# Kernel optimization log

Measured on AMD Instinct MI355X. Metric: run time of the kernel, lower is better.

The kernel has to match this reference:

```python
import jax, jax.numpy as jnp
import numpy as np

C = 10      # output (digit) capsules
L = 16      # output capsule dim
ROUTING = 3
EPS = 1e-7  # keras backend epsilon


def squash(s):
    # n^2/(1+n^2)/(n+eps) * s, norm over last axis
    n = jnp.linalg.norm(s, axis=-1, keepdims=True)
    return (n ** 2) / (1.0 + n ** 2) / (n + EPS) * s


def setup_inputs() -> dict:
    key = jax.random.key(0)
    k1, k2 = jax.random.split(key)
    B, H, W_, iC, iL = 128, 12, 12, 32, 8
    N = H * W_ * iC  # 4608
    inputs = jax.random.normal(k1, (B, H, W_, iC, iL), dtype=jnp.float32)
    W = jax.random.normal(k2, (N, iL, L * C), dtype=jnp.float32) * 0.05
    biases = jnp.zeros((C, L), dtype=jnp.float32)
    return {"inputs": inputs, "W": W, "biases": biases}


def reference(inputs, W, biases):
    B = inputs.shape[0]
    N = W.shape[0]
    x = inputs.reshape(B, N, -1)                      # [B, N, input_L]
    u = jnp.einsum('bnj,njk->bnk', x, W)              # [B, N, C*L]
    u = u.reshape(B, N, C, L)
    b = jnp.zeros((B, N, C, 1), dtype=u.dtype)
    v = None
    for r in range(ROUTING):
        c = jax.nn.softmax(b, axis=2)                 # over output capsules
        s = jnp.sum(u * c, axis=1, keepdims=True)     # [B, 1, C, L]
        s = s + biases
        v = squash(s)
        if r < ROUTING - 1:
            b = b + jnp.sum(u * v, axis=-1, keepdims=True)
    return v[:, 0]                                    # [B, C, L]
```

## Files before the change

### kernel.cpp

```cpp
#include <hip/hip_runtime.h>
#include <math.h>


namespace {
constexpr int B_   = 128;
constexpr int N_   = 4608;
constexpr int C_   = 10;
constexpr int L_   = 16;
constexpr int CL   = C_ * L_;
constexpr int NCHK = 384;
constexpr int TILE_N = N_ / NCHK;
constexpr int BCL  = B_ * CL;
constexpr int RED_G = 16;
constexpr int RED_K = NCHK / RED_G;
constexpr int WBLK = (N_ * CL) / 256;
constexpr int XBLK = (B_ * N_) / 256;
}

typedef _Float16 h2  __attribute__((ext_vector_type(2)));
typedef _Float16 v4h __attribute__((ext_vector_type(4)));
typedef _Float16 v8h __attribute__((ext_vector_type(8)));
typedef float    v4f __attribute__((ext_vector_type(4)));

__device__ inline h2 pkrtz(float a, float b) {
  return __builtin_bit_cast(h2, __builtin_amdgcn_cvt_pkrtz(a, b));
}

#if defined(__has_builtin)
#if __has_builtin(__builtin_amdgcn_fdot2)
#define HAVE_FDOT2 1
#endif
#endif

__device__ inline float fdot2(h2 a, h2 b, float c) {
#ifdef HAVE_FDOT2
  return __builtin_amdgcn_fdot2(a, b, c, false);
#else
  return c + (float)a[0] * (float)b[0] + (float)a[1] * (float)b[1];
#endif
}

__global__ __launch_bounds__(256)
void conv_pack(const float* __restrict__ W, const float* __restrict__ x,
               v8h* __restrict__ Wt, v8h* __restrict__ xh)
{
  if ((int)blockIdx.x < WBLK) {
    const int t  = blockIdx.x * 256 + threadIdx.x;
    const int n  = t / CL, cl = t % CL;
    const float* p = W + (size_t)n * (8 * CL) + cl;
    v8h o;
#pragma unroll
    for (int j = 0; j < 8; ++j) o[j] = (_Float16)p[j * CL];
    Wt[t] = o;
  } else {
    const int t = ((int)blockIdx.x - WBLK) * 256 + threadIdx.x;
    const float4 a = ((const float4*)x)[(size_t)t * 2 + 0];
    const float4 b = ((const float4*)x)[(size_t)t * 2 + 1];
    v8h o = { (_Float16)a.x, (_Float16)a.y, (_Float16)a.z, (_Float16)a.w,
              (_Float16)b.x, (_Float16)b.y, (_Float16)b.z, (_Float16)b.w };
    xh[t] = o;
  }
}

template<int MODE>
__global__ __launch_bounds__(256, 3)
void pass_kernel(const _Float16* __restrict__ xh,
                 const _Float16* __restrict__ Wt,
                 const float* __restrict__ va,
                 const float* __restrict__ vb,
                 float* __restrict__ partials)
{
  const int lane = threadIdx.x & 63;
  const int wid  = threadIdx.x >> 6;
  const int bl   = lane & 15;
  const int hi   = lane >> 4;
  const int b    = blockIdx.y * 64 + wid * 16 + bl;
  const int n0   = blockIdx.x * TILE_N;
  const int joff = (hi & 1) * 4;
  const int noff = (MODE == 0) ? (hi >> 1) : 0;
  const bool lo  = lane < 32;

  h2 vvh[C_][2];
  if (MODE >= 1) {
#pragma unroll
    for (int c = 0; c < C_; ++c) {
      v4f t = *(const v4f*)(va + ((size_t)b * C_ + c) * L_ + hi * 4);
      if (MODE == 2)
        t += *(const v4f*)(vb + ((size_t)b * C_ + c) * L_ + hi * 4);
      vvh[c][0] = pkrtz(t[0], t[1]);
      vvh[c][1] = pkrtz(t[2], t[3]);
    }
  }

  const v4f zf = {0.f, 0.f, 0.f, 0.f};
  v4f sacc[C_];
#pragma unroll
  for (int c = 0; c < C_; ++c) sacc[c] = zf;

  const _Float16* xp = xh + ((size_t)b * N_ + n0 + noff) * 8 + joff;
  const _Float16* wp = Wt + ((size_t)(n0 + noff) * CL + bl) * 8 + joff;

  constexpr int NSTEP = (MODE == 0) ? 2 : 1;
  for (int nn = 0; nn < TILE_N; nn += NSTEP) {
    v4h xf = *(const v4h*)(xp + nn * 8);
    v4h wf[C_];
#pragma unroll
    for (int c = 0; c < C_; ++c)
      wf[c] = *(const v4h*)(wp + (size_t)nn * (CL * 8) + c * (16 * 8));

    if (MODE == 0) {
#pragma unroll
      for (int c = 0; c < C_; ++c)
        sacc[c] = __builtin_amdgcn_mfma_f32_16x16x16f16(wf[c], xf, sacc[c], 0, 0, 0);
    } else {
      v4h xm = xf;
      if (!lo) { v4h z = {}; xm = z; }

      float tt[C_];
#pragma unroll
      for (int c = 0; c < C_; ++c) {
        const v4f u = __builtin_amdgcn_mfma_f32_16x16x16f16(wf[c], xm, zf, 0, 0, 0);
        const h2 ua = pkrtz(u[0], u[1]);
        const h2 ub = pkrtz(u[2], u[3]);
        float t = fdot2(ua, vvh[c][0], 0.f);
        tt[c] = fdot2(ub, vvh[c][1], t);
      }
#pragma unroll
      for (int c = 0; c < C_; ++c) {
        tt[c] += __shfl_xor(tt[c], 16);
        tt[c] += __shfl_xor(tt[c], 32);
      }
      float es = 0.f;
#pragma unroll
      for (int c = 0; c < C_; ++c) { tt[c] = __expf(tt[c]); es += tt[c]; }
      const float rs = __builtin_amdgcn_rcpf(es);

#pragma unroll
      for (int c = 0; c < C_; ++c) {
        const _Float16 wh = (_Float16)(tt[c] * rs);
        const v4h xw = xm * wh;
        sacc[c] = __builtin_amdgcn_mfma_f32_16x16x16f16(wf[c], xw, sacc[c], 0, 0, 0);
      }
    }
  }

  float* pout = partials + ((size_t)blockIdx.x * B_ + b) * CL + hi * 4;
#pragma unroll
  for (int c = 0; c < C_; ++c)
    *(v4f*)(pout + c * L_) = sacc[c];
}

__global__ __launch_bounds__(256)
void reduce_a(const float* __restrict__ p, float* __restrict__ p2) {
  const int t   = blockIdx.x * 256 + threadIdx.x;
  const int idx = t % BCL;
  const int g   = t / BCL;
  float a = 0.f;
#pragma unroll
  for (int k = 0; k < RED_K; ++k)
    a += p[(size_t)(g * RED_K + k) * BCL + idx];
  p2[t] = a;
}

__global__ __launch_bounds__(256)
void reduce_b(const float* __restrict__ p2, const float* __restrict__ biases,
              float* __restrict__ vout, float scale) {
  const int idx = blockIdx.x * 256 + threadIdx.x;
  float a = 0.f;
#pragma unroll
  for (int g = 0; g < RED_G; ++g) a += p2[(size_t)g * BCL + idx];
  const float s = a * scale + biases[idx % CL];
  float n2 = s * s;
#pragma unroll
  for (int o = 8; o; o >>= 1) n2 += __shfl_xor(n2, o, 16);
  const float n = sqrtf(n2);
  const float f = n2 / ((1.f + n2) * (n + 1e-7f));
  vout[idx] = f * s;
}

extern "C" void kernel_launch(void* const* d_in, const int* in_sizes, int n_in,
                              void* d_out, int out_size, void* d_ws, size_t ws_size,
                              hipStream_t stream) {
  const float* x      = (const float*)d_in[0];
  const float* W      = (const float*)d_in[1];
  const float* biases = (const float*)d_in[2];
  float* out = (float*)d_out;

  _Float16* Wt  = (_Float16*)d_ws;
  _Float16* xhp = Wt + (size_t)N_ * CL * 8 + 64;
  float* partials = (float*)(xhp + (size_t)B_ * N_ * 8 + 64);
  float* p2 = partials + (size_t)NCHK * BCL;
  float* v0 = p2 + (size_t)RED_G * BCL;
  float* v1 = v0 + BCL;

  conv_pack<<<WBLK + XBLK, 256, 0, stream>>>(W, x, (v8h*)Wt, (v8h*)xhp);

  const dim3 pg(NCHK, 2), pb(256);

  pass_kernel<0><<<pg, pb, 0, stream>>>(xhp, Wt, nullptr, nullptr, partials);
  reduce_a<<<(RED_G * BCL) / 256, 256, 0, stream>>>(partials, p2);
  reduce_b<<<BCL / 256, 256, 0, stream>>>(p2, biases, v0, 0.1f);

  pass_kernel<1><<<pg, pb, 0, stream>>>(xhp, Wt, v0, nullptr, partials);
  reduce_a<<<(RED_G * BCL) / 256, 256, 0, stream>>>(partials, p2);
  reduce_b<<<BCL / 256, 256, 0, stream>>>(p2, biases, v1, 1.0f);

  pass_kernel<2><<<pg, pb, 0, stream>>>(xhp, Wt, v0, v1, partials);
  reduce_a<<<(RED_G * BCL) / 256, 256, 0, stream>>>(partials, p2);
  reduce_b<<<BCL / 256, 256, 0, stream>>>(p2, biases, out, 1.0f);
}
```

Baseline: 184.1 us.

## Split N across waves within block and reduce partials through LDS

Each block now covers 16 batch rows, and its four waves each process a separate 6-element slice of N. The per-wave accumulators are summed through padded shared memory before one partial write per block. This halves the number of N chunks and the partial-sum traffic going to the reduction kernels, and raises the occupancy hint. In exchange, W reuse across batch within a block drops, so there are more W reads from cache, plus an LDS reduction and a barrier. The softmax denominator sum is also restructured as a tree.

```diff
diff --git a/kernel.cpp b/kernel.cpp
--- a/kernel.cpp
+++ b/kernel.cpp
@@ -8,13 +8,15 @@
 constexpr int C_   = 10;
 constexpr int L_   = 16;
 constexpr int CL   = C_ * L_;
-constexpr int NCHK = 384;
-constexpr int TILE_N = N_ / NCHK;
+constexpr int TILE_W = 6;
+constexpr int TILE_B = 4 * TILE_W;
+constexpr int NCHK = N_ / TILE_B;
 constexpr int BCL  = B_ * CL;
 constexpr int RED_G = 16;
 constexpr int RED_K = NCHK / RED_G;
 constexpr int WBLK = (N_ * CL) / 256;
 constexpr int XBLK = (B_ * N_) / 256;
+constexpr int PADL = 164;
 }
 
 typedef _Float16 h2  __attribute__((ext_vector_type(2)));
@@ -63,19 +65,21 @@
 }
 
 template<int MODE>
-__global__ __launch_bounds__(256, 3)
+__global__ __launch_bounds__(256, 4)
 void pass_kernel(const _Float16* __restrict__ xh,
                  const _Float16* __restrict__ Wt,
                  const float* __restrict__ va,
                  const float* __restrict__ vb,
                  float* __restrict__ partials)
 {
+  __shared__ float red[3 * 16 * PADL];
+
   const int lane = threadIdx.x & 63;
   const int wid  = threadIdx.x >> 6;
   const int bl   = lane & 15;
   const int hi   = lane >> 4;
-  const int b    = blockIdx.y * 64 + wid * 16 + bl;
-  const int n0   = blockIdx.x * TILE_N;
+  const int b    = blockIdx.y * 16 + bl;
+  const int n0   = blockIdx.x * TILE_B + wid * TILE_W;
   const int joff = (hi & 1) * 4;
   const int noff = (MODE == 0) ? (hi >> 1) : 0;
   const bool lo  = lane < 32;
@@ -101,7 +105,7 @@
   const _Float16* wp = Wt + ((size_t)(n0 + noff) * CL + bl) * 8 + joff;
 
   constexpr int NSTEP = (MODE == 0) ? 2 : 1;
-  for (int nn = 0; nn < TILE_N; nn += NSTEP) {
+  for (int nn = 0; nn < TILE_W; nn += NSTEP) {
     v4h xf = *(const v4h*)(xp + nn * 8);
     v4h wf[C_];
 #pragma unroll
@@ -130,9 +134,12 @@
         tt[c] += __shfl_xor(tt[c], 16);
         tt[c] += __shfl_xor(tt[c], 32);
       }
-      float es = 0.f;
-#pragma unroll
-      for (int c = 0; c < C_; ++c) { tt[c] = __expf(tt[c]); es += tt[c]; }
+#pragma unroll
+      for (int c = 0; c < C_; ++c) tt[c] = __expf(tt[c]);
+      float e01 = tt[0] + tt[1], e23 = tt[2] + tt[3];
+      float e45 = tt[4] + tt[5], e67 = tt[6] + tt[7];
+      float e89 = tt[8] + tt[9];
+      const float es = ((e01 + e23) + (e45 + e67)) + e89;
       const float rs = __builtin_amdgcn_rcpf(es);
 
 #pragma unroll
@@ -144,10 +151,24 @@
     }
   }
 
-  float* pout = partials + ((size_t)blockIdx.x * B_ + b) * CL + hi * 4;
-#pragma unroll
-  for (int c = 0; c < C_; ++c)
-    *(v4f*)(pout + c * L_) = sacc[c];
+  if (wid > 0) {
+    float* dst = &red[(wid - 1) * 16 * PADL + bl * PADL];
+#pragma unroll
+    for (int c = 0; c < C_; ++c)
+      *(v4f*)(dst + c * 16 + hi * 4) = sacc[c];
+  }
+  __syncthreads();
+  if (wid == 0) {
+    float* pout = partials + ((size_t)blockIdx.x * B_ + b) * CL + hi * 4;
+#pragma unroll
+    for (int c = 0; c < C_; ++c) {
+      v4f a = sacc[c];
+#pragma unroll
+      for (int s = 0; s < 3; ++s)
+        a += *(const v4f*)(&red[s * 16 * PADL + bl * PADL + c * 16 + hi * 4]);
+      *(v4f*)(pout + c * L_) = a;
+    }
+  }
 }
 
 __global__ __launch_bounds__(256)
@@ -195,7 +216,7 @@
 
   conv_pack<<<WBLK + XBLK, 256, 0, stream>>>(W, x, (v8h*)Wt, (v8h*)xhp);
 
-  const dim3 pg(NCHK, 2), pb(256);
+  const dim3 pg(NCHK, 8), pb(256);
 
   pass_kernel<0><<<pg, pb, 0, stream>>>(xhp, Wt, nullptr, nullptr, partials);
   reduce_a<<<(RED_G * BCL) / 256, 256, 0, stream>>>(partials, p2);
```

New measurement: 189.3 us. 2.8% more time.

## Stage W and x tiles into LDS via global_load_lds before routing loop

Applied to the files above, without the earlier changes.

Each pass block now copies its whole W tile and x tile from global memory into shared memory using direct global-to-LDS loads, synchronises once, then reads operands from LDS inside the loop instead of issuing strided global loads. The change also turns the softmax denominator into a tree sum to shorten the dependency chain. This trades roughly 40KB of LDS per block, which may cut occupancy below the launch-bounds target, and adds an up-front load phase that the compute does not overlap.

```diff
diff --git a/kernel.cpp b/kernel.cpp
--- a/kernel.cpp
+++ b/kernel.cpp
@@ -15,6 +15,8 @@
 constexpr int RED_K = NCHK / RED_G;
 constexpr int WBLK = (N_ * CL) / 256;
 constexpr int XBLK = (B_ * N_) / 256;
+constexpr int WI   = TILE_N * CL * 8 * 2 / 1024;
+constexpr int XI   = TILE_N * 64 * 8 * 2 / 1024;
 }
 
 typedef _Float16 h2  __attribute__((ext_vector_type(2)));
@@ -39,6 +41,11 @@
   return c + (float)a[0] * (float)b[0] + (float)a[1] * (float)b[1];
 #endif
 }
+
+#define GL2LDS(gsrc, ldsbase)                                               \
+  __builtin_amdgcn_global_load_lds(                                         \
+      (const __attribute__((address_space(1))) void*)(gsrc),                \
+      (__attribute__((address_space(3))) void*)(ldsbase), 16, 0, 0)
 
 __global__ __launch_bounds__(256)
 void conv_pack(const float* __restrict__ W, const float* __restrict__ x,
@@ -70,15 +77,30 @@
                  const float* __restrict__ vb,
                  float* __restrict__ partials)
 {
+  __shared__ __align__(16) _Float16 w_lds[TILE_N * CL * 8];
+  __shared__ __align__(16) _Float16 x_lds[TILE_N * 64 * 8];
+
   const int lane = threadIdx.x & 63;
   const int wid  = threadIdx.x >> 6;
   const int bl   = lane & 15;
   const int hi   = lane >> 4;
-  const int b    = blockIdx.y * 64 + wid * 16 + bl;
+  const int bbase = blockIdx.y * 64;
+  const int b    = bbase + wid * 16 + bl;
   const int n0   = blockIdx.x * TILE_N;
   const int joff = (hi & 1) * 4;
   const int noff = (MODE == 0) ? (hi >> 1) : 0;
   const bool lo  = lane < 32;
+
+  for (int i = wid; i < WI + XI; i += 4) {
+    if (i < WI) {
+      const _Float16* g = Wt + (size_t)n0 * CL * 8 + (size_t)i * 512 + lane * 8;
+      GL2LDS(g, w_lds + i * 512);
+    } else {
+      const int i2 = i - WI;
+      const _Float16* g = xh + ((size_t)(bbase + lane) * N_ + n0 + i2) * 8;
+      GL2LDS(g, x_lds + i2 * 512);
+    }
+  }
 
   h2 vvh[C_][2];
   if (MODE >= 1) {
@@ -97,16 +119,19 @@
 #pragma unroll
   for (int c = 0; c < C_; ++c) sacc[c] = zf;
 
-  const _Float16* xp = xh + ((size_t)b * N_ + n0 + noff) * 8 + joff;
-  const _Float16* wp = Wt + ((size_t)(n0 + noff) * CL + bl) * 8 + joff;
+  __syncthreads();
+
+  const _Float16* xrow = x_lds + (wid * 16 + bl) * 8 + joff;
+  const _Float16* wrow = w_lds + bl * 8 + joff;
 
   constexpr int NSTEP = (MODE == 0) ? 2 : 1;
   for (int nn = 0; nn < TILE_N; nn += NSTEP) {
-    v4h xf = *(const v4h*)(xp + nn * 8);
+    const int na = nn + noff;
+    v4h xf = *(const v4h*)(xrow + (size_t)na * (64 * 8));
     v4h wf[C_];
 #pragma unroll
     for (int c = 0; c < C_; ++c)
-      wf[c] = *(const v4h*)(wp + (size_t)nn * (CL * 8) + c * (16 * 8));
+      wf[c] = *(const v4h*)(wrow + ((size_t)na * CL + c * 16) * 8);
 
     if (MODE == 0) {
 #pragma unroll
@@ -130,9 +155,12 @@
         tt[c] += __shfl_xor(tt[c], 16);
         tt[c] += __shfl_xor(tt[c], 32);
       }
-      float es = 0.f;
-#pragma unroll
-      for (int c = 0; c < C_; ++c) { tt[c] = __expf(tt[c]); es += tt[c]; }
+#pragma unroll
+      for (int c = 0; c < C_; ++c) tt[c] = __expf(tt[c]);
+      float e01 = tt[0] + tt[1], e23 = tt[2] + tt[3];
+      float e45 = tt[4] + tt[5], e67 = tt[6] + tt[7];
+      float e89 = tt[8] + tt[9];
+      const float es = ((e01 + e23) + (e45 + e67)) + e89;
       const float rs = __builtin_amdgcn_rcpf(es);
 
 #pragma unroll
```

New measurement: 173.8 us. 1.06x faster.
